# Optimization experiments

Hardware: AMD Instinct MI355X
Metric: run time of the kernel (lower is better)

Reference implementation:

```python
import jax, jax.numpy as jnp
import numpy as np

N = 4194304
EPS = 1e-6


def setup_inputs() -> dict:
    key = jax.random.key(0)
    k1, k2, k3, k4 = jax.random.split(key, 4)
    # valid xyxy boxes: top-left in [0,100), positive width/height in (0,50)
    pxy = jax.random.uniform(k1, (N, 2), jnp.float32) * 100.0
    pwh = jax.random.uniform(k2, (N, 2), jnp.float32) * 50.0 + 1e-3
    txy = jax.random.uniform(k3, (N, 2), jnp.float32) * 100.0
    twh = jax.random.uniform(k4, (N, 2), jnp.float32) * 50.0 + 1e-3
    predictions = jnp.concatenate([pxy, pxy + pwh], axis=1)
    targets = jnp.concatenate([txy, txy + twh], axis=1)
    return {"predictions": predictions, "targets": targets}


def reference(predictions, targets):
    loss_weight = 1.0
    p, t = predictions, targets
    # paired IoU (diagonal of the pairwise matrix in the original == elementwise)
    area_p = (p[:, 2] - p[:, 0]) * (p[:, 3] - p[:, 1])
    area_t = (t[:, 2] - t[:, 0]) * (t[:, 3] - t[:, 1])
    lt_i = jnp.maximum(p[:, :2], t[:, :2])
    rb_i = jnp.minimum(p[:, 2:], t[:, 2:])
    wh_i = jnp.clip(rb_i - lt_i, 0.0)
    inter = wh_i[:, 0] * wh_i[:, 1]
    union = area_p + area_t - inter
    iou = inter / jnp.maximum(union, EPS)

    # center distance
    pred_cx = (p[:, 0] + p[:, 2]) * 0.5
    pred_cy = (p[:, 1] + p[:, 3]) * 0.5
    tgt_cx = (t[:, 0] + t[:, 2]) * 0.5
    tgt_cy = (t[:, 1] + t[:, 3]) * 0.5
    center_distance = (pred_cx - tgt_cx) ** 2 + (pred_cy - tgt_cy) ** 2

    # enclosing-box diagonal
    lt_e = jnp.minimum(p[:, :2], t[:, :2])
    rb_e = jnp.maximum(p[:, 2:], t[:, 2:])
    diagonal_distance = (rb_e[:, 0] - lt_e[:, 0]) ** 2 + (rb_e[:, 1] - lt_e[:, 1]) ** 2

    # aspect-ratio consistency term
    pred_w = p[:, 2] - p[:, 0]
    pred_h = p[:, 3] - p[:, 1]
    tgt_w = t[:, 2] - t[:, 0]
    tgt_h = t[:, 3] - t[:, 1]
    v = (4.0 / jnp.pi ** 2) * (
        jnp.arctan(tgt_w / jnp.maximum(tgt_h, EPS))
        - jnp.arctan(pred_w / jnp.maximum(pred_h, EPS))
    ) ** 2
    alpha = jax.lax.stop_gradient(v / (1.0 - iou + v + EPS))

    ciou = iou - center_distance / jnp.maximum(diagonal_distance, EPS) + alpha * v
    loss = 1.0 - ciou
    return (loss * loss_weight).mean()
```

## Files before the change

kernel.cpp:

```cpp
#include <hip/hip_runtime.h>
#include <math.h>


#define EPS 1e-6f
#define NTHREADS 256

__global__ __launch_bounds__(NTHREADS) void ciou_partial_kernel(
    const float4* __restrict__ pred,
    const float4* __restrict__ tgt,
    float* __restrict__ partials,
    int n)
{
    const float inv_pi2_4 = 4.0f / (float)(M_PI * M_PI);
    int i = blockIdx.x * NTHREADS + threadIdx.x;

    float acc = 0.0f;
    if (i < n) {
        float4 p = pred[i];
        float4 t = tgt[i];

        float pw = p.z - p.x, ph = p.w - p.y;
        float tw = t.z - t.x, th = t.w - t.y;
        float area_p = pw * ph;
        float area_t = tw * th;

        float ix = fminf(p.z, t.z) - fmaxf(p.x, t.x);
        float iy = fminf(p.w, t.w) - fmaxf(p.y, t.y);
        ix = fmaxf(ix, 0.0f);
        iy = fmaxf(iy, 0.0f);
        float inter = ix * iy;
        float uni = area_p + area_t - inter;
        float iou = inter / fmaxf(uni, EPS);

        float dcx = 0.5f * ((p.x + p.z) - (t.x + t.z));
        float dcy = 0.5f * ((p.y + p.w) - (t.y + t.w));
        float center_d = dcx * dcx + dcy * dcy;

        float ex = fmaxf(p.z, t.z) - fminf(p.x, t.x);
        float ey = fmaxf(p.w, t.w) - fminf(p.y, t.y);
        float diag_d = ex * ex + ey * ey;

        float num = tw * ph - pw * th;
        float den = th * ph + tw * pw;
        float da = atanf(num / den);
        float v = inv_pi2_4 * da * da;
        float alpha = v / (1.0f - iou + v + EPS);

        float ciou = iou - center_d / fmaxf(diag_d, EPS) + alpha * v;
        acc = 1.0f - ciou;
    }

    #pragma unroll
    for (int off = 32; off > 0; off >>= 1)
        acc += __shfl_down(acc, off, 64);

    __shared__ float wsum[NTHREADS / 64];
    int lane = threadIdx.x & 63;
    int wid  = threadIdx.x >> 6;
    if (lane == 0) wsum[wid] = acc;
    __syncthreads();
    if (threadIdx.x == 0) {
        float b = wsum[0];
        #pragma unroll
        for (int w = 1; w < NTHREADS / 64; ++w) b += wsum[w];
        partials[blockIdx.x] = b;
    }
}

__global__ __launch_bounds__(NTHREADS) void ciou_finalize_kernel(
    const float* __restrict__ partials, float* __restrict__ out, int nblocks, float inv_n)
{
    double acc = 0.0;
    for (int i = threadIdx.x; i < nblocks; i += NTHREADS)
        acc += (double)partials[i];

    #pragma unroll
    for (int off = 32; off > 0; off >>= 1)
        acc += __shfl_down(acc, off, 64);

    __shared__ double wsum[NTHREADS / 64];
    int lane = threadIdx.x & 63;
    int wid  = threadIdx.x >> 6;
    if (lane == 0) wsum[wid] = acc;
    __syncthreads();
    if (threadIdx.x == 0) {
        double b = wsum[0];
        #pragma unroll
        for (int w = 1; w < NTHREADS / 64; ++w) b += wsum[w];
        out[0] = (float)(b * (double)inv_n);
    }
}

extern "C" void kernel_launch(void* const* d_in, const int* in_sizes, int n_in,
                              void* d_out, int out_size, void* d_ws, size_t ws_size,
                              hipStream_t stream)
{
    const float4* pred = (const float4*)d_in[0];
    const float4* tgt  = (const float4*)d_in[1];
    int n = in_sizes[0] / 4;
    int nblocks = (n + NTHREADS - 1) / NTHREADS;

    float* partials = (float*)d_ws;
    float* out = (float*)d_out;

    ciou_partial_kernel<<<nblocks, NTHREADS, 0, stream>>>(pred, tgt, partials, n);
    ciou_finalize_kernel<<<1, NTHREADS, 0, stream>>>(partials, out, nblocks, 1.0f / (float)n);
}
```

Measured before the change: 156.8 us.

## Process four boxes per thread with inline-asm loads and staged waitcnt

Each thread now handles four box pairs strided across the grid. All eight 16-byte loads are issued up front with inline assembly, and s_waitcnt fences let compute on the first pairs overlap with the loads still in flight. The grid shrinks by four, which cuts the number of block partials and the reduction overhead. The fast path only runs when n is exactly stride*4, otherwise a grid-stride fallback loop is used. Hand-written asm loads and sched barriers can limit compiler scheduling and raise register pressure.

Measured after the change: 152.8 us. 1.03x faster.

```diff
diff --git a/kernel.cpp b/kernel.cpp
--- a/kernel.cpp
+++ b/kernel.cpp
@@ -4,6 +4,51 @@
 
 #define EPS 1e-6f
 #define NTHREADS 256
+#define PER_THREAD 4
+
+__device__ __forceinline__ float ciou_loss(float4 p, float4 t)
+{
+    const float inv_pi2_4 = 4.0f / (float)(M_PI * M_PI);
+
+    float pw = p.z - p.x, ph = p.w - p.y;
+    float tw = t.z - t.x, th = t.w - t.y;
+    float area_p = pw * ph;
+    float area_t = tw * th;
+
+    float ix = fminf(p.z, t.z) - fmaxf(p.x, t.x);
+    float iy = fminf(p.w, t.w) - fmaxf(p.y, t.y);
+    ix = fmaxf(ix, 0.0f);
+    iy = fmaxf(iy, 0.0f);
+    float inter = ix * iy;
+    float uni = area_p + area_t - inter;
+    float iou = inter / fmaxf(uni, EPS);
+
+    float dcx = 0.5f * ((p.x + p.z) - (t.x + t.z));
+    float dcy = 0.5f * ((p.y + p.w) - (t.y + t.w));
+    float center_d = dcx * dcx + dcy * dcy;
+
+    float ex = fmaxf(p.z, t.z) - fminf(p.x, t.x);
+    float ey = fmaxf(p.w, t.w) - fminf(p.y, t.y);
+    float diag_d = ex * ex + ey * ey;
+
+    float num = tw * ph - pw * th;
+    float den = th * ph + tw * pw;
+    float da = atanf(num / den);
+    float v = inv_pi2_4 * da * da;
+    float alpha = v / (1.0f - iou + v + EPS);
+
+    float ciou = iou - center_d / fmaxf(diag_d, EPS) + alpha * v;
+    return 1.0f - ciou;
+}
+
+#define ASM_LOAD(dst, addr) \
+    asm volatile("global_load_dwordx4 %0, %1, off" : "=&v"(dst) : "v"(addr) : "memory")
+
+#define WAITCNT_FENCE(N)                                        \
+    do {                                                        \
+        asm volatile("s_waitcnt vmcnt(" #N ")" ::: "memory");   \
+        __builtin_amdgcn_sched_barrier(0);                      \
+    } while (0)
 
 __global__ __launch_bounds__(NTHREADS) void ciou_partial_kernel(
     const float4* __restrict__ pred,
@@ -11,43 +56,35 @@
     float* __restrict__ partials,
     int n)
 {
-    const float inv_pi2_4 = 4.0f / (float)(M_PI * M_PI);
-    int i = blockIdx.x * NTHREADS + threadIdx.x;
+    float acc;
+    const int tid = blockIdx.x * NTHREADS + threadIdx.x;
+    const int stride = gridDim.x * NTHREADS;
 
-    float acc = 0.0f;
-    if (i < n) {
-        float4 p = pred[i];
-        float4 t = tgt[i];
+    if (n == stride * PER_THREAD) {
+        float4 p0, p1, p2, p3, t0, t1, t2, t3;
+        ASM_LOAD(p0, pred + tid + 0 * stride);
+        ASM_LOAD(t0, tgt  + tid + 0 * stride);
+        ASM_LOAD(p1, pred + tid + 1 * stride);
+        ASM_LOAD(t1, tgt  + tid + 1 * stride);
+        ASM_LOAD(p2, pred + tid + 2 * stride);
+        ASM_LOAD(t2, tgt  + tid + 2 * stride);
+        ASM_LOAD(p3, pred + tid + 3 * stride);
+        ASM_LOAD(t3, tgt  + tid + 3 * stride);
 
-        float pw = p.z - p.x, ph = p.w - p.y;
-        float tw = t.z - t.x, th = t.w - t.y;
-        float area_p = pw * ph;
-        float area_t = tw * th;
-
-        float ix = fminf(p.z, t.z) - fmaxf(p.x, t.x);
-        float iy = fminf(p.w, t.w) - fmaxf(p.y, t.y);
-        ix = fmaxf(ix, 0.0f);
-        iy = fmaxf(iy, 0.0f);
-        float inter = ix * iy;
-        float uni = area_p + area_t - inter;
-        float iou = inter / fmaxf(uni, EPS);
-
-        float dcx = 0.5f * ((p.x + p.z) - (t.x + t.z));
-        float dcy = 0.5f * ((p.y + p.w) - (t.y + t.w));
-        float center_d = dcx * dcx + dcy * dcy;
-
-        float ex = fmaxf(p.z, t.z) - fminf(p.x, t.x);
-        float ey = fmaxf(p.w, t.w) - fminf(p.y, t.y);
-        float diag_d = ex * ex + ey * ey;
-
-        float num = tw * ph - pw * th;
-        float den = th * ph + tw * pw;
-        float da = atanf(num / den);
-        float v = inv_pi2_4 * da * da;
-        float alpha = v / (1.0f - iou + v + EPS);
-
-        float ciou = iou - center_d / fmaxf(diag_d, EPS) + alpha * v;
-        acc = 1.0f - ciou;
+        float acc0 = 0.0f, acc1 = 0.0f;
+        WAITCNT_FENCE(6);
+        acc0 += ciou_loss(p0, t0);
+        WAITCNT_FENCE(4);
+        acc1 += ciou_loss(p1, t1);
+        WAITCNT_FENCE(2);
+        acc0 += ciou_loss(p2, t2);
+        WAITCNT_FENCE(0);
+        acc1 += ciou_loss(p3, t3);
+        acc = acc0 + acc1;
+    } else {
+        acc = 0.0f;
+        for (int i = tid; i < n; i += stride)
+            acc += ciou_loss(pred[i], tgt[i]);
     }
 
     #pragma unroll
@@ -98,7 +135,7 @@
     const float4* pred = (const float4*)d_in[0];
     const float4* tgt  = (const float4*)d_in[1];
     int n = in_sizes[0] / 4;
-    int nblocks = (n + NTHREADS - 1) / NTHREADS;
+    int nblocks = (n + NTHREADS * PER_THREAD - 1) / (NTHREADS * PER_THREAD);
 
     float* partials = (float*)d_ws;
     float* out = (float*)d_out;
```
